# Optimization experiments

Hardware: AMD Instinct MI355X
Metric: run time of the kernel (lower is better)

The kernel has to match this reference:

```python
import jax, jax.numpy as jnp
import numpy as np

NEG_INF = -9e15  # matches torch's -9000000000000000.0 mask value
ALPHA = 0.2      # LeakyReLU negative slope


def setup_inputs() -> dict:
    key = jax.random.key(0)
    k1, k2, k3, k4 = jax.random.split(key, 4)
    B, N, Fin, Fout = 8, 2048, 256, 256
    h = jax.random.normal(k1, (B, N, Fin), dtype=jnp.float32)
    adj = jax.random.randint(k2, (B, N, N), 0, 2, dtype=jnp.int32)
    # xavier_uniform with gain=1.414
    limW = 1.414 * np.sqrt(6.0 / (Fin + Fout))
    W = jax.random.uniform(k3, (Fin, Fout), minval=-limW, maxval=limW, dtype=jnp.float32)
    lima = 1.414 * np.sqrt(6.0 / (2 * Fout + 1))
    a = jax.random.uniform(k4, (2 * Fout, 1), minval=-lima, maxval=lima, dtype=jnp.float32)
    return {"h": h, "adj": adj, "W": W, "a": a}


def reference(h, adj, W, a):
    # h: (B, N, Fin), adj: (B, N, N), W: (Fin, Fout), a: (2*Fout, 1)
    Fout = W.shape[1]
    Wh = jnp.einsum('bni,io->bno', h, W)                 # (B, N, Fout)
    # e[b,i,j] = leakyrelu(Wh[b,i] @ a1 + Wh[b,j] @ a2) -- equivalent to the
    # original concat([Wh_i, Wh_j]) @ a without the O(N^2 * 2F) intermediate.
    e1 = Wh @ a[:Fout, 0]                                # (B, N)
    e2 = Wh @ a[Fout:, 0]                                # (B, N)
    e = jax.nn.leaky_relu(e1[:, :, None] + e2[:, None, :], negative_slope=ALPHA)
    masked = jnp.where(adj > 0, e, NEG_INF)
    attention = jax.nn.softmax(masked, axis=-1)          # (B, N, N)
    # dropout omitted (deterministic eval-mode reference)
    h_prime = jnp.einsum('bij,bjo->bio', attention, Wh)  # (B, N, Fout)
    return jax.nn.elu(h_prime), attention
```

## Files before the change

### kernel.cpp

```cpp
#include <hip/hip_runtime.h>
#include <hip/hip_bf16.h>
#include <stdint.h>

#define NEG_INF -9.0e15f
#define LRELU_ALPHA 0.2f

using bf16x8  = __attribute__((ext_vector_type(8))) short;
using f32x4   = __attribute__((ext_vector_type(4))) float;
using short4v = __attribute__((ext_vector_type(4))) short;
using int4v   = __attribute__((ext_vector_type(4))) int;
using float4v = __attribute__((ext_vector_type(4))) float;

static __device__ __forceinline__ float b2f(short s) {
  unsigned u = ((unsigned)(unsigned short)s) << 16;
  return __builtin_bit_cast(float, u);
}
static __device__ __forceinline__ short f2bf(float f) {
  unsigned u = __builtin_bit_cast(unsigned, f);
  u = u + 0x7FFFu + ((u >> 16) & 1u);
  return (short)(u >> 16);
}
static __device__ __forceinline__ void gload16(const void* g, void* l) {
  __builtin_amdgcn_global_load_lds((const __attribute__((address_space(1))) void*)g,
                                   (__attribute__((address_space(3))) void*)l, 16, 0, 0);
}

__global__ __launch_bounds__(256) void cast_f32_bf16_kernel(
    const float* __restrict__ src, short* __restrict__ dst, int n)
{
  int i0 = (blockIdx.x * 256 + threadIdx.x) * 8;
  if (i0 >= n) return;
  float4v v0 = *(const float4v*)(src + i0);
  float4v v1 = *(const float4v*)(src + i0 + 4);
  short os[8] __attribute__((aligned(16)));
#pragma unroll
  for (int k = 0; k < 8; ++k) {
    float x = (k < 4) ? v0[k] : v1[k - 4];
    x = (x - x == 0.0f) ? x : 0.0f;
    os[k] = f2bf(x);
  }
  *(int4v*)(dst + i0) = *(const int4v*)os;
}

__global__ __launch_bounds__(256) void transpose_bf16_kernel(
    const short* __restrict__ src, short* __restrict__ dst,
    int M, int N, long long ss, long long ds)
{
  __shared__ short t[64][68];
  const int b = blockIdx.z;
  src += (long long)b * ss; dst += (long long)b * ds;
  const int m0 = blockIdx.x * 64, n0 = blockIdx.y * 64;
  const int tid = threadIdx.x;
  const int rr = tid >> 3, cc = (tid & 7) * 8;
#pragma unroll
  for (int p = 0; p < 2; ++p) {
    int row = rr + p * 32;
    const short* sp = src + (long long)(m0 + row) * N + n0 + cc;
    short4v v0 = *(const short4v*)sp;
    short4v v1 = *(const short4v*)(sp + 4);
    *(short4v*)&t[row][cc]     = v0;
    *(short4v*)&t[row][cc + 4] = v1;
  }
  __syncthreads();
#pragma unroll
  for (int p = 0; p < 2; ++p) {
    int orow = rr + p * 32;
    short vv[8] __attribute__((aligned(16)));
#pragma unroll
    for (int j = 0; j < 8; ++j) vv[j] = t[cc + j][orow];
    short* dp = dst + (long long)(n0 + orow) * M + m0 + cc;
    *(int4v*)dp = *(const int4v*)vv;
  }
}

__global__ __launch_bounds__(256) void evec_kernel(
    const short* __restrict__ Wh, const float* __restrict__ a,
    float* __restrict__ e1, float* __restrict__ e2)
{
  const int wid = threadIdx.x >> 6, lane = threadIdx.x & 63;
  const long long r = (long long)blockIdx.x * 4 + wid;
  short4v hv   = *(const short4v*)(Wh + r * 256 + lane * 4);
  float4v a1v  = *(const float4v*)(a + lane * 4);
  float4v a2v  = *(const float4v*)(a + 256 + lane * 4);
  float s1 = 0.f, s2 = 0.f;
#pragma unroll
  for (int k = 0; k < 4; ++k) {
    float x = b2f(hv[k]);
    s1 += x * a1v[k];
    s2 += x * a2v[k];
  }
#pragma unroll
  for (int off = 32; off > 0; off >>= 1) {
    s1 += __shfl_xor(s1, off, 64);
    s2 += __shfl_xor(s2, off, 64);
  }
  if (lane == 0) { e1[r] = s1; e2[r] = s2; }
}

__global__ __launch_bounds__(256) void attn_softmax_kernel(
    const int* __restrict__ adj, const float* __restrict__ e1,
    const float* __restrict__ e2, float* __restrict__ attn)
{
  const int i = blockIdx.x;
  const int b = blockIdx.y;
  const long long row = (long long)b * 2048 + i;
  const int tid = threadIdx.x;
  const int wid = tid >> 6, lane = tid & 63;
  const int j0 = tid * 8;

  const int*   arow = adj + row * 2048 + j0;
  const float  ei   = e1[row];
  const float* e2b  = e2 + b * 2048 + j0;

  int4v   a0 = *(const int4v*)(arow);
  int4v   a1 = *(const int4v*)(arow + 4);
  float4v f0 = *(const float4v*)(e2b);
  float4v f1 = *(const float4v*)(e2b + 4);

  float s[8];
#pragma unroll
  for (int k = 0; k < 8; ++k) {
    float x = ei + (k < 4 ? f0[k] : f1[k - 4]);
    float v = x > 0.f ? x : LRELU_ALPHA * x;
    int  ad = (k < 4 ? a0[k] : a1[k - 4]);
    s[k] = (ad > 0) ? v : NEG_INF;
  }
  float m = s[0];
#pragma unroll
  for (int k = 1; k < 8; ++k) m = fmaxf(m, s[k]);
#pragma unroll
  for (int off = 32; off > 0; off >>= 1) m = fmaxf(m, __shfl_xor(m, off, 64));

  __shared__ float wmax[4], wsum[4];
  if (lane == 0) wmax[wid] = m;
  __syncthreads();
  const float M = fmaxf(fmaxf(wmax[0], wmax[1]), fmaxf(wmax[2], wmax[3]));

  float p[8]; float t = 0.f;
#pragma unroll
  for (int k = 0; k < 8; ++k) { p[k] = __expf(s[k] - M); t += p[k]; }
#pragma unroll
  for (int off = 32; off > 0; off >>= 1) t += __shfl_xor(t, off, 64);
  if (lane == 0) wsum[wid] = t;
  __syncthreads();
  const float S = wsum[0] + wsum[1] + wsum[2] + wsum[3];
  const float r = 1.0f / S;

  float4v o0, o1;
#pragma unroll
  for (int k = 0; k < 4; ++k) { o0[k] = p[k] * r; o1[k] = p[k + 4] * r; }
  float* op = attn + row * 2048 + j0;
  *(float4v*)op       = o0;
  *(float4v*)(op + 4) = o1;
}

__global__ __launch_bounds__(256) void gemm_bt(
    const short* __restrict__ A, const short* __restrict__ Bt,
    short* __restrict__ C, int N, int K)
{
  __shared__ short As[128 * 32];
  __shared__ short Bs[128 * 32];
  const int m0 = blockIdx.x * 128, n0 = blockIdx.y * 128;
  const int tid = threadIdx.x;
  const int w = tid >> 6, lane = tid & 63;
  const int wr = w >> 1, wc = w & 1;
  const int g = lane >> 4, lr = lane & 15;

  f32x4 acc[4][4] = {};

  for (int k0 = 0; k0 < K; k0 += 32) {
    __syncthreads();
#pragma unroll
    for (int q = 0; q < 2; ++q) {
      int p = w * 2 + q;
      int c = p * 64 + lane;
      int row = c >> 2, kq = (c & 3) << 3;
      gload16(A  + (long long)(m0 + row) * K + k0 + kq, As + p * 512);
      gload16(Bt + (long long)(n0 + row) * K + k0 + kq, Bs + p * 512);
    }
    __syncthreads();

    bf16x8 af[4], bfr[4];
#pragma unroll
    for (int i = 0; i < 4; ++i) {
      af[i]  = *(const bf16x8*)(As + (wr * 64 + i * 16 + lr) * 32 + 8 * g);
      bfr[i] = *(const bf16x8*)(Bs + (wc * 64 + i * 16 + lr) * 32 + 8 * g);
    }
#pragma unroll
    for (int i = 0; i < 4; ++i)
#pragma unroll
      for (int j = 0; j < 4; ++j)
        acc[i][j] = __builtin_amdgcn_mfma_f32_16x16x32_bf16(af[i], bfr[j], acc[i][j], 0, 0, 0);
  }

#pragma unroll
  for (int i = 0; i < 4; ++i) {
    int row_base = m0 + wr * 64 + i * 16 + 4 * g;
#pragma unroll
    for (int j = 0; j < 4; ++j) {
      int col = n0 + wc * 64 + j * 16 + lr;
#pragma unroll
      for (int r = 0; r < 4; ++r)
        C[(long long)(row_base + r) * N + col] = f2bf(acc[i][j][r]);
    }
  }
}

__global__ __launch_bounds__(256, 4) void gemm_attn_kernel(
    const float* __restrict__ A, const short* __restrict__ Bt,
    float* __restrict__ C)
{
  __shared__ short As[32 * 64];
  __shared__ short Bs[256 * 64];
  const int bz = blockIdx.z;
  A  += (long long)bz * 4194304;
  Bt += (long long)bz * 524288;
  C  += (long long)bz * 524288;
  const int m0 = blockIdx.x * 32;
  const int tid = threadIdx.x;
  const int w = tid >> 6, lane = tid & 63;
  const int g = lane >> 4, lr = lane & 15;

  f32x4 acc[2][4] = {};

  const int ar = tid >> 3, ac8 = tid & 7;
  short* as_wr = As + ar * 64 + ((ac8 ^ (ar & 7)) << 3);
  const float* a_rd_base = A + (long long)(m0 + ar) * 2048 + ac8 * 8;

  const int bcol_off = lane >> 3;
  const int bchunk   = (lane & 7) ^ ((lane >> 3) & 7);

  for (int k0 = 0; k0 < 2048; k0 += 64) {
    __syncthreads();
    {
      const float* ap = a_rd_base + k0;
      float4v u0 = *(const float4v*)ap;
      float4v u1 = *(const float4v*)(ap + 4);
      short os[8] __attribute__((aligned(16)));
#pragma unroll
      for (int k = 0; k < 8; ++k) os[k] = f2bf(k < 4 ? u0[k] : u1[k - 4]);
      *(bf16x8*)as_wr = *(const bf16x8*)os;
    }
#pragma unroll
    for (int q = 0; q < 8; ++q) {
      int p = w * 8 + q;
      int col = p * 8 + bcol_off;
      gload16(Bt + (long long)col * 2048 + k0 + bchunk * 8, Bs + p * 512);
    }
    __syncthreads();

    bf16x8 af[2][2], bfr[4][2];
#pragma unroll
    for (int i = 0; i < 2; ++i) {
      int row = i * 16 + lr;
#pragma unroll
      for (int s = 0; s < 2; ++s)
        af[i][s] = *(const bf16x8*)(As + row * 64 + (((s * 4 + g) ^ (row & 7)) << 3));
    }
#pragma unroll
    for (int j = 0; j < 4; ++j) {
      int col = w * 64 + j * 16 + lr;
#pragma unroll
      for (int s = 0; s < 2; ++s)
        bfr[j][s] = *(const bf16x8*)(Bs + col * 64 + (((s * 4 + g) ^ (col & 7)) << 3));
    }
#pragma unroll
    for (int s = 0; s < 2; ++s)
#pragma unroll
      for (int i = 0; i < 2; ++i)
#pragma unroll
        for (int j = 0; j < 4; ++j)
          acc[i][j] = __builtin_amdgcn_mfma_f32_16x16x32_bf16(af[i][s], bfr[j][s], acc[i][j], 0, 0, 0);
  }

#pragma unroll
  for (int i = 0; i < 2; ++i) {
    int row_base = m0 + i * 16 + 4 * g;
#pragma unroll
    for (int j = 0; j < 4; ++j) {
      int col = w * 64 + j * 16 + lr;
#pragma unroll
      for (int r = 0; r < 4; ++r) {
        float v = acc[i][j][r];
        v = (v > 0.f) ? v : (__expf(v) - 1.f);
        C[(long long)(row_base + r) * 256 + col] = v;
      }
    }
  }
}

extern "C" void kernel_launch(void* const* d_in, const int* in_sizes, int n_in,
                              void* d_out, int out_size, void* d_ws, size_t ws_size,
                              hipStream_t stream)
{
  const float* h   = (const float*)d_in[0];
  const int*   adj = (const int*)d_in[1];
  const float* W   = (const float*)d_in[2];
  const float* a   = (const float*)d_in[3];

  float* hp_out   = (float*)d_out;
  float* attn_out = hp_out + 4194304LL;

  short* h_bf = (short*)d_ws;
  short* W_bf = h_bf + 4194304;
  short* W_t  = W_bf + 65536;
  short* Wh   = W_t + 65536;
  short* Wh_t = Wh + 4194304;
  float* e1   = (float*)(Wh_t + 4194304);
  float* e2   = e1 + 16384;

  cast_f32_bf16_kernel<<<2048, 256, 0, stream>>>(h, h_bf, 4194304);
  cast_f32_bf16_kernel<<<32, 256, 0, stream>>>(W, W_bf, 65536);
  transpose_bf16_kernel<<<dim3(4, 4, 1), 256, 0, stream>>>(W_bf, W_t, 256, 256, 0, 0);
  gemm_bt<<<dim3(128, 2, 1), 256, 0, stream>>>(h_bf, W_t, Wh, 256, 256);
  transpose_bf16_kernel<<<dim3(32, 4, 8), 256, 0, stream>>>(Wh, Wh_t, 2048, 256, 524288LL, 524288LL);
  evec_kernel<<<4096, 256, 0, stream>>>(Wh, a, e1, e2);
  attn_softmax_kernel<<<dim3(2048, 8), 256, 0, stream>>>(adj, e1, e2, attn_out);
  gemm_attn_kernel<<<dim3(64, 1, 8), 256, 0, stream>>>(attn_out, Wh_t, hp_out);
}
```

Measured before the change: 127.8 us.

## Load fp32 attention tiles directly to LDS and convert to bf16 on read

The attention GEMM now copies fp32 attention tiles straight into LDS with global_load_lds instead of loading them into registers, converting to bf16, and storing. Conversion moves to the LDS read side using the packed v_cvt_pk_bf16_f32 instruction, with a 16-chunk XOR swizzle for the fp32 layout. The grid is flattened so consecutive blocks cover different batches, and launch bounds drop to 2 waves per SIMD. The A tile in LDS doubles in size, which can lower occupancy, and every wave now repeats the conversion work.

```diff
diff --git a/kernel.cpp b/kernel.cpp
--- a/kernel.cpp
+++ b/kernel.cpp
@@ -10,6 +10,7 @@
 using short4v = __attribute__((ext_vector_type(4))) short;
 using int4v   = __attribute__((ext_vector_type(4))) int;
 using float4v = __attribute__((ext_vector_type(4))) float;
+using uint4v  = __attribute__((ext_vector_type(4))) unsigned;
 
 static __device__ __forceinline__ float b2f(short s) {
   unsigned u = ((unsigned)(unsigned short)s) << 16;
@@ -19,6 +20,11 @@
   unsigned u = __builtin_bit_cast(unsigned, f);
   u = u + 0x7FFFu + ((u >> 16) & 1u);
   return (short)(u >> 16);
+}
+static __device__ __forceinline__ unsigned cvtpk_bf16(float lo, float hi) {
+  unsigned r;
+  asm volatile("v_cvt_pk_bf16_f32 %0, %1, %2" : "=v"(r) : "v"(lo), "v"(hi));
+  return r;
 }
 static __device__ __forceinline__ void gload16(const void* g, void* l) {
   __builtin_amdgcn_global_load_lds((const __attribute__((address_space(1))) void*)g,
@@ -206,41 +212,35 @@
   }
 }
 
-__global__ __launch_bounds__(256, 4) void gemm_attn_kernel(
+__global__ __launch_bounds__(256, 2) void gemm_attn_kernel(
     const float* __restrict__ A, const short* __restrict__ Bt,
     float* __restrict__ C)
 {
-  __shared__ short As[32 * 64];
+  __shared__ float As[32 * 64];
   __shared__ short Bs[256 * 64];
-  const int bz = blockIdx.z;
+  const int bid = blockIdx.x;
+  const int bz = bid & 7;
+  const int m0 = (bid >> 3) << 5;
   A  += (long long)bz * 4194304;
   Bt += (long long)bz * 524288;
   C  += (long long)bz * 524288;
-  const int m0 = blockIdx.x * 32;
   const int tid = threadIdx.x;
   const int w = tid >> 6, lane = tid & 63;
   const int g = lane >> 4, lr = lane & 15;
 
   f32x4 acc[2][4] = {};
 
-  const int ar = tid >> 3, ac8 = tid & 7;
-  short* as_wr = As + ar * 64 + ((ac8 ^ (ar & 7)) << 3);
-  const float* a_rd_base = A + (long long)(m0 + ar) * 2048 + ac8 * 8;
-
   const int bcol_off = lane >> 3;
   const int bchunk   = (lane & 7) ^ ((lane >> 3) & 7);
+  const int as_s0  = w * 128 + lane;
+  const int ar0    = as_s0 >> 4,  ac0 = as_s0 & 15;
+  const int as_s1  = as_s0 + 64;
+  const int ar1    = as_s1 >> 4,  ac1 = as_s1 & 15;
 
   for (int k0 = 0; k0 < 2048; k0 += 64) {
     __syncthreads();
-    {
-      const float* ap = a_rd_base + k0;
-      float4v u0 = *(const float4v*)ap;
-      float4v u1 = *(const float4v*)(ap + 4);
-      short os[8] __attribute__((aligned(16)));
-#pragma unroll
-      for (int k = 0; k < 8; ++k) os[k] = f2bf(k < 4 ? u0[k] : u1[k - 4]);
-      *(bf16x8*)as_wr = *(const bf16x8*)os;
-    }
+    gload16(A + (long long)(m0 + ar0) * 2048 + k0 + ((ac0 ^ (ar0 & 15)) << 2), As + as_s0 * 4);
+    gload16(A + (long long)(m0 + ar1) * 2048 + k0 + ((ac1 ^ (ar1 & 15)) << 2), As + as_s1 * 4);
 #pragma unroll
     for (int q = 0; q < 8; ++q) {
       int p = w * 8 + q;
@@ -253,9 +253,19 @@
 #pragma unroll
     for (int i = 0; i < 2; ++i) {
       int row = i * 16 + lr;
-#pragma unroll
-      for (int s = 0; s < 2; ++s)
-        af[i][s] = *(const bf16x8*)(As + row * 64 + (((s * 4 + g) ^ (row & 7)) << 3));
+      const float* arow = As + row * 64;
+#pragma unroll
+      for (int s = 0; s < 2; ++s) {
+        int ch = s * 4 + g;
+        float4v lo = *(const float4v*)(arow + (((2 * ch)     ^ (row & 15)) << 2));
+        float4v hi = *(const float4v*)(arow + (((2 * ch + 1) ^ (row & 15)) << 2));
+        uint4v uv;
+        uv[0] = cvtpk_bf16(lo[0], lo[1]);
+        uv[1] = cvtpk_bf16(lo[2], lo[3]);
+        uv[2] = cvtpk_bf16(hi[0], hi[1]);
+        uv[3] = cvtpk_bf16(hi[2], hi[3]);
+        af[i][s] = __builtin_bit_cast(bf16x8, uv);
+      }
     }
 #pragma unroll
     for (int j = 0; j < 4; ++j) {
@@ -316,5 +326,5 @@
   transpose_bf16_kernel<<<dim3(32, 4, 8), 256, 0, stream>>>(Wh, Wh_t, 2048, 256, 524288LL, 524288LL);
   evec_kernel<<<4096, 256, 0, stream>>>(Wh, a, e1, e2);
   attn_softmax_kernel<<<dim3(2048, 8), 256, 0, stream>>>(adj, e1, e2, attn_out);
-  gemm_attn_kernel<<<dim3(64, 1, 8), 256, 0, stream>>>(attn_out, Wh_t, hp_out);
-}
+  gemm_attn_kernel<<<512, 256, 0, stream>>>(attn_out, Wh_t, hp_out);
+}
```

Result: faster. 118.4 us (-7.3%).
